# Performance work log

Measured on AMD Instinct MI355X. Metric: run time of the kernel, lower is better.

## Reference

```python
import jax, jax.numpy as jnp
import numpy as np

B, C, W, H, HEADS = 32, 512, 32, 32, 8
D = C // HEADS
N = W * H
LN_EPS = 1e-5


def setup_inputs() -> dict:
    key = jax.random.key(0)
    ks = jax.random.split(key, 11)
    s = 1.0 / np.sqrt(C)
    return {
        "x": jax.random.normal(ks[0], (B, C, W, H), jnp.float32),
        "Wq": jax.random.normal(ks[1], (C, C), jnp.float32) * s,
        "bq": jax.random.normal(ks[2], (C,), jnp.float32) * 0.01,
        "Wk": jax.random.normal(ks[3], (C, C), jnp.float32) * s,
        "bk": jax.random.normal(ks[4], (C,), jnp.float32) * 0.01,
        "Wv": jax.random.normal(ks[5], (C, C), jnp.float32) * s,
        "bv": jax.random.normal(ks[6], (C,), jnp.float32) * 0.01,
        "rel_h": jax.random.normal(ks[7], (1, HEADS, D, 1, H), jnp.float32),
        "rel_w": jax.random.normal(ks[8], (1, HEADS, D, W, 1), jnp.float32),
        "ln_w": jnp.ones((C, W, H), jnp.float32),
        "ln_b": jnp.zeros((C, W, H), jnp.float32),
    }


def reference(x, Wq, bq, Wk, bk, Wv, bv, rel_h, rel_w, ln_w, ln_b):
    b, c, w, h = x.shape
    nh, d, n = HEADS, c // HEADS, w * h

    def proj(Wm, bm):
        # 1x1 conv == per-pixel linear: out[b,o,w,h] = sum_c Wm[o,c] x[b,c,w,h] + bm[o]
        y = jnp.einsum('bcwh,oc->bowh', x, Wm) + bm[None, :, None, None]
        return y.reshape(b, nh, d, n)

    q = proj(Wq, bq)  # [B,h,d,N]
    k = proj(Wk, bk)
    v = proj(Wv, bv)

    # content-content: q^T k -> [B,h,N,N]
    cc = jnp.einsum('bhdn,bhdm->bhnm', q, k)
    # content-position: (rel_h + rel_w) flattened to [h,d,N], permuted, matmul with q
    pos = (rel_h + rel_w).reshape(nh, d, n)  # [h,d,N]
    cp = jnp.einsum('hdn,bhdm->bhnm', pos, q)

    attn = jax.nn.softmax(cc + cp, axis=-1)  # [B,h,N,N]
    # out = v @ attn^T  -> [B,h,d,N]
    out = jnp.einsum('bhdn,bhmn->bhdm', v, attn)
    out = out.reshape(b, c, w, h)

    # LayerNorm over [C,W,H] with elementwise affine, then residual
    mu = jnp.mean(out, axis=(1, 2, 3), keepdims=True)
    var = jnp.var(out, axis=(1, 2, 3), keepdims=True)
    out = (out - mu) * jax.lax.rsqrt(var + LN_EPS) * ln_w[None] + ln_b[None]
    return out + x
```

## Files before the change

### kernel.cpp

```cpp
#include <hip/hip_runtime.h>
#include <stdint.h>

typedef _Float16 f16x8 __attribute__((ext_vector_type(8)));
typedef _Float16 f16x4 __attribute__((ext_vector_type(4)));
typedef __fp16   fp16x2 __attribute__((ext_vector_type(2)));
typedef float f32x4  __attribute__((ext_vector_type(4)));

__device__ __forceinline__ _Float16 f2h(float f){ return (_Float16)f; }

#define NB   32
#define NC   512
#define NH   8
#define ND   64
#define NN   1024

__global__ __launch_bounds__(256) void wt_conv(const float* __restrict__ Wq,
                                               const float* __restrict__ Wk,
                                               const float* __restrict__ Wv,
                                               _Float16* __restrict__ Wt){
  int idx = blockIdx.x * 256 + threadIdx.x;
  int sel = idx >> 18;
  const float* W = (sel == 0) ? Wq : (sel == 1) ? Wk : Wv;
  Wt[idx] = f2h(W[idx & 262143]);
}

__global__ __launch_bounds__(256) void transpose_x(const float* __restrict__ x,
                                                   _Float16* __restrict__ xT){
  __shared__ float tile[32][33];
  int n0 = blockIdx.x * 32, c0 = blockIdx.y * 32, b = blockIdx.z;
  int t = threadIdx.x;
  int tn = t & 31, tc = t >> 5;
#pragma unroll
  for (int k = 0; k < 4; k++)
    tile[tc + 8*k][tn] = x[(b*NC + c0 + tc + 8*k)*NN + n0 + tn];
  __syncthreads();
#pragma unroll
  for (int k = 0; k < 4; k++)
    xT[(b*NN + n0 + tc + 8*k)*NC + c0 + tn] = f2h(tile[tn][tc + 8*k]);
}

__global__ __launch_bounds__(256) void pos_conv(const float* __restrict__ rel_h,
                                                const float* __restrict__ rel_w,
                                                _Float16* __restrict__ pos_t){
  int idx = blockIdx.x * 256 + threadIdx.x;
  int d = idx & 63, n = (idx >> 6) & 1023, h = idx >> 16;
  int ww = n >> 5, hh = n & 31;
  float v = rel_h[(h*ND + d)*32 + hh] + rel_w[(h*ND + d)*32 + ww];
  pos_t[idx] = f2h(v);
}

#define ASTR 72
#define TSTR 136

__global__ __launch_bounds__(256) void proj_gemm(const _Float16* __restrict__ Wt,
                                                 const _Float16* __restrict__ xT,
                                                 const float* __restrict__ bq,
                                                 const float* __restrict__ bk,
                                                 const float* __restrict__ bv,
                                                 _Float16* __restrict__ q_ws,
                                                 _Float16* __restrict__ k_ws,
                                                 _Float16* __restrict__ v_ws){
  __shared__ _Float16 smem[2 * 128 * ASTR];
  _Float16* As = smem;
  _Float16* Bs = smem + 128 * ASTR;

  int mt = blockIdx.x;
  int nt = blockIdx.y;
  int b  = blockIdx.z;
  int t = threadIdx.x, lane = t & 63, w = t >> 6;
  int wm = w >> 1, wn = w & 1;
  int lr = lane & 15, lg = lane >> 4;

  f32x4 acc[4][4];
#pragma unroll
  for (int i = 0; i < 4; i++)
#pragma unroll
    for (int j = 0; j < 4; j++) acc[i][j] = (f32x4)0.f;

  const _Float16* Arow = Wt + mt * 128 * NC;
  const _Float16* Brow = xT + (b * NN + nt * 128) * NC;

  for (int k0 = 0; k0 < NC; k0 += 64){
    __syncthreads();
#pragma unroll
    for (int i = 0; i < 4; i++){
      int lin = t + 256 * i;
      int row = lin >> 3, c8 = lin & 7;
      *(f16x8*)(As + row*ASTR + c8*8) = *(const f16x8*)(Arow + row*NC + k0 + c8*8);
      *(f16x8*)(Bs + row*ASTR + c8*8) = *(const f16x8*)(Brow + row*NC + k0 + c8*8);
    }
    __syncthreads();
#pragma unroll
    for (int ks = 0; ks < 2; ks++){
      f16x8 af[4], bfr[4];
#pragma unroll
      for (int mi = 0; mi < 4; mi++)
        af[mi] = *(f16x8*)(As + (wm*64 + mi*16 + lr)*ASTR + ks*32 + lg*8);
#pragma unroll
      for (int nj = 0; nj < 4; nj++)
        bfr[nj] = *(f16x8*)(Bs + (wn*64 + nj*16 + lr)*ASTR + ks*32 + lg*8);
#pragma unroll
      for (int mi = 0; mi < 4; mi++)
#pragma unroll
        for (int nj = 0; nj < 4; nj++)
          acc[mi][nj] = __builtin_amdgcn_mfma_f32_16x16x32_f16(af[mi], bfr[nj], acc[mi][nj], 0, 0, 0);
    }
  }
  __syncthreads();

  if (mt < 8){
    _Float16* Ts = smem;
#pragma unroll
    for (int mi = 0; mi < 4; mi++){
      int o0 = wm*64 + mi*16 + 4*lg;
      int og = mt*128 + o0;
      int sel = og >> 9, oo = og & 511;
      const float* bias = (sel == 0) ? bq : bk;
      float b0 = bias[oo], b1 = bias[oo+1], b2 = bias[oo+2], b3 = bias[oo+3];
#pragma unroll
      for (int nj = 0; nj < 4; nj++){
        int pix = wn*64 + nj*16 + lr;
        f16x4 pk;
        pk[0] = f2h(acc[mi][nj][0] + b0);
        pk[1] = f2h(acc[mi][nj][1] + b1);
        pk[2] = f2h(acc[mi][nj][2] + b2);
        pk[3] = f2h(acc[mi][nj][3] + b3);
        *(f16x4*)(Ts + pix*TSTR + o0) = pk;
      }
    }
    __syncthreads();
#pragma unroll
    for (int i = 0; i < 8; i++){
      int lin = t + 256 * i;
      int c_o = lin & 15, pix = lin >> 4;
      f16x8 v = *(f16x8*)(Ts + pix*TSTR + c_o*8);
      int og = mt*128 + c_o*8;
      int sel = og >> 9, oo = og & 511;
      int head = oo >> 6, d = oo & 63;
      _Float16* dst = (sel == 0) ? q_ws : k_ws;
      *(f16x8*)(dst + (((b*NH + head)*NN) + nt*128 + pix)*ND + d) = v;
    }
  } else {
    _Float16* Ts2 = smem;
#pragma unroll
    for (int mi = 0; mi < 4; mi++){
      int o0 = wm*64 + mi*16 + 4*lg;
      int vb = (mt - 8)*128 + o0;
      float b0 = bv[vb], b1 = bv[vb+1], b2 = bv[vb+2], b3 = bv[vb+3];
#pragma unroll
      for (int nj = 0; nj < 4; nj++){
        int pix = wn*64 + nj*16 + lr;
        Ts2[(o0+0)*TSTR + pix] = f2h(acc[mi][nj][0] + b0);
        Ts2[(o0+1)*TSTR + pix] = f2h(acc[mi][nj][1] + b1);
        Ts2[(o0+2)*TSTR + pix] = f2h(acc[mi][nj][2] + b2);
        Ts2[(o0+3)*TSTR + pix] = f2h(acc[mi][nj][3] + b3);
      }
    }
    __syncthreads();
#pragma unroll
    for (int i = 0; i < 8; i++){
      int lin = t + 256 * i;
      int pix8 = lin & 15, o_loc = lin >> 4;
      f16x8 v = *(f16x8*)(Ts2 + o_loc*TSTR + pix8*8);
      int vb = (mt - 8)*128 + o_loc;
      int head = vb >> 6, d = vb & 63;
      *(f16x8*)(v_ws + ((b*NH + head)*ND + d)*NN + nt*128 + pix8*8) = v;
    }
  }
}

#define KSTR 136
#define PSTR 72
#define OSTR 65
#define OFF_VT 9216

__global__ __launch_bounds__(256) void attn_kernel(const _Float16* __restrict__ q_ws,
                                                   const _Float16* __restrict__ k_ws,
                                                   const _Float16* __restrict__ v_ws,
                                                   const _Float16* __restrict__ pos_t,
                                                   float* __restrict__ out,
                                                   float* __restrict__ red){
  __shared__ _Float16 smem[13312];
  __shared__ float lnred[8];
  _Float16* Kc = smem;
  _Float16* Pl = smem;
  _Float16* Vt = smem + OFF_VT;

  int bid = blockIdx.x;
  int sid = (bid & 7) * 256 + (bid >> 3);
  int qt = sid & 7, h = (sid >> 3) & 7, b = sid >> 6;

  int t = threadIdx.x, lane = t & 63, w = t >> 6;
  int lr = lane & 15, lg = lane >> 4;

  const _Float16* qbh = q_ws + (b*NH + h) * NN * ND;
  const _Float16* kbh = k_ws + (b*NH + h) * NN * ND;
  const _Float16* vbh = v_ws + (b*NH + h) * ND * NN;
  const _Float16* pph = pos_t + h * NN * ND;

  f16x8 qreg[2][4];
#pragma unroll
  for (int qi = 0; qi < 2; qi++){
    int row = qt*128 + w*32 + qi*16 + lr;
#pragma unroll
    for (int ks = 0; ks < 4; ks++){
      const _Float16* src = (ks < 2) ? (qbh + row*ND + ks*32 + lg*8)
                                     : (pph + row*ND + (ks-2)*32 + lg*8);
      qreg[qi][ks] = *(const f16x8*)src;
    }
  }

  float m_r[2], l_r[2];
  f32x4 oacc[2][4];
#pragma unroll
  for (int qi = 0; qi < 2; qi++){ m_r[qi] = -1e30f; l_r[qi] = 0.f; }
#pragma unroll
  for (int qi = 0; qi < 2; qi++)
#pragma unroll
    for (int dj = 0; dj < 4; dj++) oacc[qi][dj] = (f32x4)0.f;

  for (int n0 = 0; n0 < NN; n0 += 64){
    __syncthreads();
#pragma unroll
    for (int i = 0; i < 4; i++){
      int lin = t + 256*i;
      int row = lin >> 4, c8 = lin & 15;
      const _Float16* src = (c8 < 8) ? (kbh + (n0 + row)*ND + c8*8)
                                     : (qbh + (n0 + row)*ND + (c8 - 8)*8);
      *(f16x8*)(Kc + row*KSTR + c8*8) = *(const f16x8*)src;
    }
#pragma unroll
    for (int i = 0; i < 2; i++){
      int lin = t + 256*i;
      int d = lin >> 3, ch = lin & 7;
      *(f16x8*)(Vt + d*64 + ((ch*8) ^ ((d & 7) << 3))) = *(const f16x8*)(vbh + d*NN + n0 + ch*8);
    }
    __syncthreads();

    f32x4 sacc[4][2];
#pragma unroll
    for (int kt = 0; kt < 4; kt++)
#pragma unroll
      for (int qi = 0; qi < 2; qi++) sacc[kt][qi] = (f32x4)0.f;
#pragma unroll
    for (int ks = 0; ks < 4; ks++){
      f16x8 kf[4];
#pragma unroll
      for (int kt = 0; kt < 4; kt++)
        kf[kt] = *(f16x8*)(Kc + (kt*16 + lr)*KSTR + ks*32 + lg*8);
#pragma unroll
      for (int kt = 0; kt < 4; kt++)
#pragma unroll
        for (int qi = 0; qi < 2; qi++)
          sacc[kt][qi] = __builtin_amdgcn_mfma_f32_16x16x32_f16(kf[kt], qreg[qi][ks], sacc[kt][qi], 0, 0, 0);
    }

    __syncthreads();

#pragma unroll
    for (int qi = 0; qi < 2; qi++){
      float m0 = fmaxf(fmaxf(sacc[0][qi][0], sacc[0][qi][1]), fmaxf(sacc[0][qi][2], sacc[0][qi][3]));
      float m1 = fmaxf(fmaxf(sacc[1][qi][0], sacc[1][qi][1]), fmaxf(sacc[1][qi][2], sacc[1][qi][3]));
      float m2 = fmaxf(fmaxf(sacc[2][qi][0], sacc[2][qi][1]), fmaxf(sacc[2][qi][2], sacc[2][qi][3]));
      float m3 = fmaxf(fmaxf(sacc[3][qi][0], sacc[3][qi][1]), fmaxf(sacc[3][qi][2], sacc[3][qi][3]));
      float mx = fmaxf(fmaxf(m0, m1), fmaxf(m2, m3));
      mx = fmaxf(mx, __shfl_xor(mx, 16));
      mx = fmaxf(mx, __shfl_xor(mx, 32));
      if (!__all(mx - m_r[qi] <= 8.f)){
        float mn = fmaxf(m_r[qi], mx);
        float cr = __expf(m_r[qi] - mn);
        m_r[qi] = mn;
        l_r[qi] *= cr;
#pragma unroll
        for (int r = 0; r < 4; r++){
          float crow = __shfl(cr, 4*lg + r);
#pragma unroll
          for (int dj = 0; dj < 4; dj++) oacc[qi][dj][r] *= crow;
        }
      }
      float mn = m_r[qi];
      float ts = 0.f;
#pragma unroll
      for (int kt = 0; kt < 4; kt++){
        float p0 = __expf(sacc[kt][qi][0] - mn);
        float p1 = __expf(sacc[kt][qi][1] - mn);
        float p2 = __expf(sacc[kt][qi][2] - mn);
        float p3 = __expf(sacc[kt][qi][3] - mn);
        ts += (p0 + p1) + (p2 + p3);
        union { fp16x2 h2[2]; uint2 u2; } pu;
        pu.h2[0] = __builtin_amdgcn_cvt_pkrtz(p0, p1);
        pu.h2[1] = __builtin_amdgcn_cvt_pkrtz(p2, p3);
        *(uint2*)(Pl + (w*32 + qi*16 + lr)*PSTR + kt*16 + lg*4) = pu.u2;
      }
      ts += __shfl_xor(ts, 16);
      ts += __shfl_xor(ts, 32);
      l_r[qi] += ts;
    }

#pragma unroll
    for (int ks = 0; ks < 2; ks++){
      f16x8 pf[2], vf[4];
#pragma unroll
      for (int qi = 0; qi < 2; qi++)
        pf[qi] = *(f16x8*)(Pl + (w*32 + qi*16 + lr)*PSTR + ks*32 + lg*8);
#pragma unroll
      for (int dj = 0; dj < 4; dj++){
        int row = dj*16 + lr;
        vf[dj] = *(f16x8*)(Vt + row*64 + ((ks*32 + lg*8) ^ ((row & 7) << 3)));
      }
#pragma unroll
      for (int qi = 0; qi < 2; qi++)
#pragma unroll
        for (int dj = 0; dj < 4; dj++)
          oacc[qi][dj] = __builtin_amdgcn_mfma_f32_16x16x32_f16(pf[qi], vf[dj], oacc[qi][dj], 0, 0, 0);
    }
  }

  float s_ln = 0.f, q_ln = 0.f;
  __syncthreads();
  float* Ot = (float*)smem;
#pragma unroll
  for (int p = 0; p < 2; p++){
    if ((w >> 1) == p){
      int wl = w & 1;
#pragma unroll
      for (int qi = 0; qi < 2; qi++){
        float iv = 1.f / l_r[qi];
#pragma unroll
        for (int r = 0; r < 4; r++){
          float invr = __shfl(iv, 4*lg + r);
#pragma unroll
          for (int dj = 0; dj < 4; dj++){
            float val = oacc[qi][dj][r] * invr;
            s_ln += val; q_ln += val*val;
            Ot[(wl*32 + qi*16 + 4*lg + r)*OSTR + dj*16 + lr] = val;
          }
        }
      }
    }
    __syncthreads();
#pragma unroll
    for (int i = 0; i < 4; i++){
      int lin = t + 256*i;
      int d = lin >> 4, jc = lin & 15;
      float4 v;
      v.x = Ot[(jc*4 + 0)*OSTR + d];
      v.y = Ot[(jc*4 + 1)*OSTR + d];
      v.z = Ot[(jc*4 + 2)*OSTR + d];
      v.w = Ot[(jc*4 + 3)*OSTR + d];
      *(float4*)(out + (b*NC + h*ND + d)*NN + qt*128 + p*64 + jc*4) = v;
    }
    __syncthreads();
  }

#pragma unroll
  for (int off = 1; off < 64; off <<= 1){
    s_ln += __shfl_xor(s_ln, off);
    q_ln += __shfl_xor(q_ln, off);
  }
  if (lane == 0){ lnred[w*2] = s_ln; lnred[w*2 + 1] = q_ln; }
  __syncthreads();
  if (t == 0){
    int idx = ((b*NH + h)*8 + qt)*2;
    red[idx]     = lnred[0] + lnred[2] + lnred[4] + lnred[6];
    red[idx + 1] = lnred[1] + lnred[3] + lnred[5] + lnred[7];
  }
}

__global__ void ln_stats(const float* __restrict__ red, float* __restrict__ stats){
  int b = threadIdx.x;
  if (b < 32){
    float s = 0.f, sq = 0.f;
    for (int j = 0; j < 64; j++){ s += red[(b*64 + j)*2]; sq += red[(b*64 + j)*2 + 1]; }
    float mu  = s * (1.f / 524288.f);
    float var = sq * (1.f / 524288.f) - mu*mu;
    stats[b*2] = mu;
    stats[b*2 + 1] = rsqrtf(var + 1e-5f);
  }
}

__global__ __launch_bounds__(256) void ln_apply(const float* __restrict__ x,
                                                const float* __restrict__ lw,
                                                const float* __restrict__ lb,
                                                const float* __restrict__ stats,
                                                float* __restrict__ out){
  int tid = blockIdx.x*256 + threadIdx.x;
  for (int i4 = tid; i4 < 4194304; i4 += 524288){
    int b = i4 >> 17;
    int r4 = i4 & 131071;
    float mu = stats[b*2], rs = stats[b*2 + 1];
    float4 o  = ((const float4*)out)[i4];
    float4 xv = ((const float4*)x)[i4];
    float4 ww = ((const float4*)lw)[r4];
    float4 bb = ((const float4*)lb)[r4];
    o.x = (o.x - mu)*rs*ww.x + bb.x + xv.x;
    o.y = (o.y - mu)*rs*ww.y + bb.y + xv.y;
    o.z = (o.z - mu)*rs*ww.z + bb.z + xv.z;
    o.w = (o.w - mu)*rs*ww.w + bb.w + xv.w;
    ((float4*)out)[i4] = o;
  }
}

extern "C" void kernel_launch(void* const* d_in, const int* in_sizes, int n_in,
                              void* d_out, int out_size, void* d_ws, size_t ws_size,
                              hipStream_t stream){
  (void)in_sizes; (void)n_in; (void)out_size; (void)ws_size;
  const float* x    = (const float*)d_in[0];
  const float* Wq   = (const float*)d_in[1];
  const float* bq   = (const float*)d_in[2];
  const float* Wk   = (const float*)d_in[3];
  const float* bk   = (const float*)d_in[4];
  const float* Wv   = (const float*)d_in[5];
  const float* bv   = (const float*)d_in[6];
  const float* relh = (const float*)d_in[7];
  const float* relw = (const float*)d_in[8];
  const float* lnw  = (const float*)d_in[9];
  const float* lnb  = (const float*)d_in[10];
  float* out = (float*)d_out;
  char* ws = (char*)d_ws;

  _Float16* q_ws  = (_Float16*)(ws);
  _Float16* k_ws  = (_Float16*)(ws + 33554432);
  _Float16* v_ws  = (_Float16*)(ws + 67108864);
  _Float16* xT    = (_Float16*)(ws + 100663296);
  _Float16* Wt    = (_Float16*)(ws + 134217728);
  _Float16* pos_t = (_Float16*)(ws + 135790592);
  float* red   = (float*)(ws + 136839168);
  float* stats = red + 4096;

  wt_conv    <<<3072, 256, 0, stream>>>(Wq, Wk, Wv, Wt);
  transpose_x<<<dim3(32, 16, 32), 256, 0, stream>>>(x, xT);
  pos_conv   <<<2048, 256, 0, stream>>>(relh, relw, pos_t);
  proj_gemm  <<<dim3(12, 8, 32), 256, 0, stream>>>(Wt, xT, bq, bk, bv, q_ws, k_ws, v_ws);
  attn_kernel<<<2048, 256, 0, stream>>>(q_ws, k_ws, v_ws, pos_t, out, red);
  ln_stats   <<<1, 64, 0, stream>>>(red, stats);
  ln_apply   <<<2048, 256, 0, stream>>>(x, lnw, lnb, stats, out);
}
```

Measured before the change: 320.9 us.

## Prefetch next K/V tile into registers and fold log2e into Q for exp2 softmax

The attention loop now loads the next 64-key K/Q/V tile into registers while the current tile is computed, then writes it to LDS at the top of the next iteration, so global latency overlaps the MFMA and softmax work. P gets its own LDS region instead of aliasing the K buffer, which removes one __syncthreads per iteration but enlarges shared memory. The Q projection output is pre-scaled by log2e so the softmax can use exp2 directly, with the rescale threshold adjusted to match. A launch-bounds occupancy hint of 3 blocks per CU is added, which may increase register pressure alongside the prefetch registers.

```diff
diff --git a/kernel.cpp b/kernel.cpp
--- a/kernel.cpp
+++ b/kernel.cpp
@@ -13,6 +13,8 @@
 #define NH   8
 #define ND   64
 #define NN   1024
+
+#define LOG2E 1.44269504f
 
 __global__ __launch_bounds__(256) void wt_conv(const float* __restrict__ Wq,
                                                const float* __restrict__ Wk,
@@ -116,15 +118,16 @@
       int og = mt*128 + o0;
       int sel = og >> 9, oo = og & 511;
       const float* bias = (sel == 0) ? bq : bk;
+      float sc = (sel == 0) ? LOG2E : 1.f;
       float b0 = bias[oo], b1 = bias[oo+1], b2 = bias[oo+2], b3 = bias[oo+3];
 #pragma unroll
       for (int nj = 0; nj < 4; nj++){
         int pix = wn*64 + nj*16 + lr;
         f16x4 pk;
-        pk[0] = f2h(acc[mi][nj][0] + b0);
-        pk[1] = f2h(acc[mi][nj][1] + b1);
-        pk[2] = f2h(acc[mi][nj][2] + b2);
-        pk[3] = f2h(acc[mi][nj][3] + b3);
+        pk[0] = f2h((acc[mi][nj][0] + b0) * sc);
+        pk[1] = f2h((acc[mi][nj][1] + b1) * sc);
+        pk[2] = f2h((acc[mi][nj][2] + b2) * sc);
+        pk[3] = f2h((acc[mi][nj][3] + b3) * sc);
         *(f16x4*)(Ts + pix*TSTR + o0) = pk;
       }
     }
@@ -172,19 +175,20 @@
 #define KSTR 136
 #define PSTR 72
 #define OSTR 65
-#define OFF_VT 9216
-
-__global__ __launch_bounds__(256) void attn_kernel(const _Float16* __restrict__ q_ws,
-                                                   const _Float16* __restrict__ k_ws,
-                                                   const _Float16* __restrict__ v_ws,
-                                                   const _Float16* __restrict__ pos_t,
-                                                   float* __restrict__ out,
-                                                   float* __restrict__ red){
-  __shared__ _Float16 smem[13312];
+#define OFF_VT 8704
+#define OFF_P  12800
+
+__global__ __launch_bounds__(256, 3) void attn_kernel(const _Float16* __restrict__ q_ws,
+                                                      const _Float16* __restrict__ k_ws,
+                                                      const _Float16* __restrict__ v_ws,
+                                                      const _Float16* __restrict__ pos_t,
+                                                      float* __restrict__ out,
+                                                      float* __restrict__ red){
+  __shared__ _Float16 smem[22016];
   __shared__ float lnred[8];
   _Float16* Kc = smem;
-  _Float16* Pl = smem;
   _Float16* Vt = smem + OFF_VT;
+  _Float16* Pl = smem + OFF_P;
 
   int bid = blockIdx.x;
   int sid = (bid & 7) * 256 + (bid >> 3);
@@ -210,6 +214,21 @@
     }
   }
 
+  int k_row = t >> 4, k_c8 = t & 15;
+  int v_d = t >> 3, v_ch = t & 7;
+
+  f16x8 kst[4], vst[2];
+#pragma unroll
+  for (int i = 0; i < 4; i++){
+    int row = k_row + i*16;
+    const _Float16* src = (k_c8 < 8) ? (kbh + row*ND + k_c8*8)
+                                     : (qbh + row*ND + (k_c8 - 8)*8);
+    kst[i] = *(const f16x8*)src;
+  }
+#pragma unroll
+  for (int i = 0; i < 2; i++)
+    vst[i] = *(const f16x8*)(vbh + (v_d + i*32)*NN + v_ch*8);
+
   float m_r[2], l_r[2];
   f32x4 oacc[2][4];
 #pragma unroll
@@ -219,21 +238,28 @@
 #pragma unroll
     for (int dj = 0; dj < 4; dj++) oacc[qi][dj] = (f32x4)0.f;
 
-  for (int n0 = 0; n0 < NN; n0 += 64){
-    __syncthreads();
-#pragma unroll
-    for (int i = 0; i < 4; i++){
-      int lin = t + 256*i;
-      int row = lin >> 4, c8 = lin & 15;
-      const _Float16* src = (c8 < 8) ? (kbh + (n0 + row)*ND + c8*8)
-                                     : (qbh + (n0 + row)*ND + (c8 - 8)*8);
-      *(f16x8*)(Kc + row*KSTR + c8*8) = *(const f16x8*)src;
-    }
+  for (int tt = 0; tt < 16; tt++){
+    __syncthreads();
+#pragma unroll
+    for (int i = 0; i < 4; i++)
+      *(f16x8*)(Kc + (k_row + i*16)*KSTR + k_c8*8) = kst[i];
 #pragma unroll
     for (int i = 0; i < 2; i++){
-      int lin = t + 256*i;
-      int d = lin >> 3, ch = lin & 7;
-      *(f16x8*)(Vt + d*64 + ((ch*8) ^ ((d & 7) << 3))) = *(const f16x8*)(vbh + d*NN + n0 + ch*8);
+      int d = v_d + i*32;
+      *(f16x8*)(Vt + d*64 + ((v_ch*8) ^ ((d & 7) << 3))) = vst[i];
+    }
+    if (tt < 15){
+      int n1 = tt*64 + 64;
+#pragma unroll
+      for (int i = 0; i < 4; i++){
+        int row = n1 + k_row + i*16;
+        const _Float16* src = (k_c8 < 8) ? (kbh + row*ND + k_c8*8)
+                                         : (qbh + row*ND + (k_c8 - 8)*8);
+        kst[i] = *(const f16x8*)src;
+      }
+#pragma unroll
+      for (int i = 0; i < 2; i++)
+        vst[i] = *(const f16x8*)(vbh + (v_d + i*32)*NN + n1 + v_ch*8);
     }
     __syncthreads();
 
@@ -254,8 +280,6 @@
         for (int qi = 0; qi < 2; qi++)
           sacc[kt][qi] = __builtin_amdgcn_mfma_f32_16x16x32_f16(kf[kt], qreg[qi][ks], sacc[kt][qi], 0, 0, 0);
     }
-
-    __syncthreads();
 
 #pragma unroll
     for (int qi = 0; qi < 2; qi++){
@@ -266,9 +290,9 @@
       float mx = fmaxf(fmaxf(m0, m1), fmaxf(m2, m3));
       mx = fmaxf(mx, __shfl_xor(mx, 16));
       mx = fmaxf(mx, __shfl_xor(mx, 32));
-      if (!__all(mx - m_r[qi] <= 8.f)){
+      if (!__all(mx - m_r[qi] <= 11.f)){
         float mn = fmaxf(m_r[qi], mx);
-        float cr = __expf(m_r[qi] - mn);
+        float cr = __builtin_exp2f(m_r[qi] - mn);
         m_r[qi] = mn;
         l_r[qi] *= cr;
 #pragma unroll
@@ -282,10 +306,10 @@
       float ts = 0.f;
 #pragma unroll
       for (int kt = 0; kt < 4; kt++){
-        float p0 = __expf(sacc[kt][qi][0] - mn);
-        float p1 = __expf(sacc[kt][qi][1] - mn);
-        float p2 = __expf(sacc[kt][qi][2] - mn);
-        float p3 = __expf(sacc[kt][qi][3] - mn);
+        float p0 = __builtin_exp2f(sacc[kt][qi][0] - mn);
+        float p1 = __builtin_exp2f(sacc[kt][qi][1] - mn);
+        float p2 = __builtin_exp2f(sacc[kt][qi][2] - mn);
+        float p3 = __builtin_exp2f(sacc[kt][qi][3] - mn);
         ts += (p0 + p1) + (p2 + p3);
         union { fp16x2 h2[2]; uint2 u2; } pu;
         pu.h2[0] = __builtin_amdgcn_cvt_pkrtz(p0, p1);
```

Measured after the change: 334.0 us. 4.1% more time.

## Fold log2e into Q, compute row sums via MFMA, split P buffer, add setprio

Applied to the files above, without the earlier changes.

Q is prescaled by log2(e) in the projection epilogue so the softmax uses exp2 directly, and the rescale threshold is adjusted to match. The row-sum of probabilities is now accumulated with an extra MFMA against a vector of ones instead of shuffle reductions. P gets its own shared-memory region, which removes one barrier per tile and lets the output epilogue write all 128 rows in one pass, at the cost of more LDS per block. It also adds s_setprio around the MFMA sections and a launch-bounds occupancy hint.

```diff
diff --git a/kernel.cpp b/kernel.cpp
--- a/kernel.cpp
+++ b/kernel.cpp
@@ -13,6 +13,8 @@
 #define NH   8
 #define ND   64
 #define NN   1024
+
+#define LOG2E 1.44269504f
 
 __global__ __launch_bounds__(256) void wt_conv(const float* __restrict__ Wq,
                                                const float* __restrict__ Wk,
@@ -116,15 +118,16 @@
       int og = mt*128 + o0;
       int sel = og >> 9, oo = og & 511;
       const float* bias = (sel == 0) ? bq : bk;
+      float sc = (sel == 0) ? LOG2E : 1.f;
       float b0 = bias[oo], b1 = bias[oo+1], b2 = bias[oo+2], b3 = bias[oo+3];
 #pragma unroll
       for (int nj = 0; nj < 4; nj++){
         int pix = wn*64 + nj*16 + lr;
         f16x4 pk;
-        pk[0] = f2h(acc[mi][nj][0] + b0);
-        pk[1] = f2h(acc[mi][nj][1] + b1);
-        pk[2] = f2h(acc[mi][nj][2] + b2);
-        pk[3] = f2h(acc[mi][nj][3] + b3);
+        pk[0] = f2h((acc[mi][nj][0] + b0) * sc);
+        pk[1] = f2h((acc[mi][nj][1] + b1) * sc);
+        pk[2] = f2h((acc[mi][nj][2] + b2) * sc);
+        pk[3] = f2h((acc[mi][nj][3] + b3) * sc);
         *(f16x4*)(Ts + pix*TSTR + o0) = pk;
       }
     }
@@ -172,19 +175,20 @@
 #define KSTR 136
 #define PSTR 72
 #define OSTR 65
-#define OFF_VT 9216
-
-__global__ __launch_bounds__(256) void attn_kernel(const _Float16* __restrict__ q_ws,
-                                                   const _Float16* __restrict__ k_ws,
-                                                   const _Float16* __restrict__ v_ws,
-                                                   const _Float16* __restrict__ pos_t,
-                                                   float* __restrict__ out,
-                                                   float* __restrict__ red){
-  __shared__ _Float16 smem[13312];
+#define OFF_VT 8704
+#define OFF_P  12800
+
+__global__ __launch_bounds__(256, 3) void attn_kernel(const _Float16* __restrict__ q_ws,
+                                                      const _Float16* __restrict__ k_ws,
+                                                      const _Float16* __restrict__ v_ws,
+                                                      const _Float16* __restrict__ pos_t,
+                                                      float* __restrict__ out,
+                                                      float* __restrict__ red){
+  __shared__ _Float16 smem[22016];
   __shared__ float lnred[8];
   _Float16* Kc = smem;
-  _Float16* Pl = smem;
   _Float16* Vt = smem + OFF_VT;
+  _Float16* Pl = smem + OFF_P;
 
   int bid = blockIdx.x;
   int sid = (bid & 7) * 256 + (bid >> 3);
@@ -210,10 +214,15 @@
     }
   }
 
-  float m_r[2], l_r[2];
+  f16x8 ones;
+#pragma unroll
+  for (int e = 0; e < 8; e++) ones[e] = (_Float16)1.f;
+
+  float m_r[2];
   f32x4 oacc[2][4];
-#pragma unroll
-  for (int qi = 0; qi < 2; qi++){ m_r[qi] = -1e30f; l_r[qi] = 0.f; }
+  f32x4 lacc[2];
+#pragma unroll
+  for (int qi = 0; qi < 2; qi++){ m_r[qi] = -1e30f; lacc[qi] = (f32x4)0.f; }
 #pragma unroll
   for (int qi = 0; qi < 2; qi++)
 #pragma unroll
@@ -242,6 +251,7 @@
     for (int kt = 0; kt < 4; kt++)
 #pragma unroll
       for (int qi = 0; qi < 2; qi++) sacc[kt][qi] = (f32x4)0.f;
+    __builtin_amdgcn_s_setprio(1);
 #pragma unroll
     for (int ks = 0; ks < 4; ks++){
       f16x8 kf[4];
@@ -254,8 +264,7 @@
         for (int qi = 0; qi < 2; qi++)
           sacc[kt][qi] = __builtin_amdgcn_mfma_f32_16x16x32_f16(kf[kt], qreg[qi][ks], sacc[kt][qi], 0, 0, 0);
     }
-
-    __syncthreads();
+    __builtin_amdgcn_s_setprio(0);
 
 #pragma unroll
     for (int qi = 0; qi < 2; qi++){
@@ -266,37 +275,33 @@
       float mx = fmaxf(fmaxf(m0, m1), fmaxf(m2, m3));
       mx = fmaxf(mx, __shfl_xor(mx, 16));
       mx = fmaxf(mx, __shfl_xor(mx, 32));
-      if (!__all(mx - m_r[qi] <= 8.f)){
-        float mn = fmaxf(m_r[qi], mx);
-        float cr = __expf(m_r[qi] - mn);
-        m_r[qi] = mn;
-        l_r[qi] *= cr;
+      if (!__all(mx - m_r[qi] <= 11.f)){
+        float mn2 = fmaxf(m_r[qi], mx);
+        float cr = __builtin_exp2f(m_r[qi] - mn2);
+        m_r[qi] = mn2;
 #pragma unroll
         for (int r = 0; r < 4; r++){
           float crow = __shfl(cr, 4*lg + r);
+          lacc[qi][r] *= crow;
 #pragma unroll
           for (int dj = 0; dj < 4; dj++) oacc[qi][dj][r] *= crow;
         }
       }
       float mn = m_r[qi];
-      float ts = 0.f;
 #pragma unroll
       for (int kt = 0; kt < 4; kt++){
-        float p0 = __expf(sacc[kt][qi][0] - mn);
-        float p1 = __expf(sacc[kt][qi][1] - mn);
-        float p2 = __expf(sacc[kt][qi][2] - mn);
-        float p3 = __expf(sacc[kt][qi][3] - mn);
-        ts += (p0 + p1) + (p2 + p3);
+        float p0 = __builtin_exp2f(sacc[kt][qi][0] - mn);
+        float p1 = __builtin_exp2f(sacc[kt][qi][1] - mn);
+        float p2 = __builtin_exp2f(sacc[kt][qi][2] - mn);
+        float p3 = __builtin_exp2f(sacc[kt][qi][3] - mn);
         union { fp16x2 h2[2]; uint2 u2; } pu;
         pu.h2[0] = __builtin_amdgcn_cvt_pkrtz(p0, p1);
         pu.h2[1] = __builtin_amdgcn_cvt_pkrtz(p2, p3);
         *(uint2*)(Pl + (w*32 + qi*16 + lr)*PSTR + kt*16 + lg*4) = pu.u2;
       }
-      ts += __shfl_xor(ts, 16);
-      ts += __shfl_xor(ts, 32);
-      l_r[qi] += ts;
-    }
-
+    }
+
+    __builtin_amdgcn_s_setprio(1);
 #pragma unroll
     for (int ks = 0; ks < 2; ks++){
       f16x8 pf[2], vf[4];
@@ -309,48 +314,44 @@
         vf[dj] = *(f16x8*)(Vt + row*64 + ((ks*32 + lg*8) ^ ((row & 7) << 3)));
       }
 #pragma unroll
-      for (int qi = 0; qi < 2; qi++)
+      for (int qi = 0; qi < 2; qi++){
+        lacc[qi] = __builtin_amdgcn_mfma_f32_16x16x32_f16(pf[qi], ones, lacc[qi], 0, 0, 0);
 #pragma unroll
         for (int dj = 0; dj < 4; dj++)
           oacc[qi][dj] = __builtin_amdgcn_mfma_f32_16x16x32_f16(pf[qi], vf[dj], oacc[qi][dj], 0, 0, 0);
-    }
+      }
+    }
+    __builtin_amdgcn_s_setprio(0);
   }
 
   float s_ln = 0.f, q_ln = 0.f;
   __syncthreads();
   float* Ot = (float*)smem;
 #pragma unroll
-  for (int p = 0; p < 2; p++){
-    if ((w >> 1) == p){
-      int wl = w & 1;
-#pragma unroll
-      for (int qi = 0; qi < 2; qi++){
-        float iv = 1.f / l_r[qi];
-#pragma unroll
-        for (int r = 0; r < 4; r++){
-          float invr = __shfl(iv, 4*lg + r);
-#pragma unroll
-          for (int dj = 0; dj < 4; dj++){
-            float val = oacc[qi][dj][r] * invr;
-            s_ln += val; q_ln += val*val;
-            Ot[(wl*32 + qi*16 + 4*lg + r)*OSTR + dj*16 + lr] = val;
-          }
-        }
-      }
-    }
-    __syncthreads();
-#pragma unroll
-    for (int i = 0; i < 4; i++){
-      int lin = t + 256*i;
-      int d = lin >> 4, jc = lin & 15;
-      float4 v;
-      v.x = Ot[(jc*4 + 0)*OSTR + d];
-      v.y = Ot[(jc*4 + 1)*OSTR + d];
-      v.z = Ot[(jc*4 + 2)*OSTR + d];
-      v.w = Ot[(jc*4 + 3)*OSTR + d];
-      *(float4*)(out + (b*NC + h*ND + d)*NN + qt*128 + p*64 + jc*4) = v;
-    }
-    __syncthreads();
+  for (int qi = 0; qi < 2; qi++){
+#pragma unroll
+    for (int r = 0; r < 4; r++){
+      float invr = 1.f / lacc[qi][r];
+#pragma unroll
+      for (int dj = 0; dj < 4; dj++){
+        float val = oacc[qi][dj][r] * invr;
+        s_ln += val; q_ln += val*val;
+        Ot[(w*32 + qi*16 + 4*lg + r)*OSTR + dj*16 + lr] = val;
+      }
+    }
+  }
+  __syncthreads();
+
+#pragma unroll
+  for (int i = 0; i < 8; i++){
+    int lin = t + 256*i;
+    int jc = lin & 31, d = lin >> 5;
+    float4 v;
+    v.x = Ot[(jc*4 + 0)*OSTR + d];
+    v.y = Ot[(jc*4 + 1)*OSTR + d];
+    v.z = Ot[(jc*4 + 2)*OSTR + d];
+    v.w = Ot[(jc*4 + 3)*OSTR + d];
+    *(float4*)(out + (b*NC + h*ND + d)*NN + qt*128 + jc*4) = v;
   }
 
 #pragma unroll
```

Result: faster. 303.3 us (-5.5%).
